# Performance work log

Measured on AMD Instinct MI355X. Metric: run time of the kernel, lower is better.

The kernel has to match this reference:

```python
import jax, jax.numpy as jnp
import numpy as np

B, S = 16, 8192
D_MODEL = 128          # config.moe_intermediate_size
D_HID = 512            # config.intermediate_size
N_EXPERTS = 8
BEH_DIM = 32           # config.behavior_embedding_dim
N_BEH = 16             # config.num_behavior -> embedding rows = N_BEH + 1


def setup_inputs() -> dict:
    key = jax.random.key(0)
    k1, k2, k3, k4, k5, k6 = jax.random.split(key, 6)
    hidden_states = jax.random.normal(k1, (B, S, D_MODEL), dtype=jnp.float32)
    position_index = jax.random.randint(k2, (B, S), 0, N_EXPERTS, dtype=jnp.int32)
    behavior_index = jax.random.randint(k3, (B, S), 0, N_BEH + 1, dtype=jnp.int32)
    din = D_MODEL + BEH_DIM
    # expert weights: wi maps (D_MODEL+BEH_DIM)->D_HID, wo maps D_HID->D_MODEL (no bias)
    Wi = jax.random.normal(k4, (N_EXPERTS, din, D_HID), dtype=jnp.float32) * (din ** -0.5)
    Wo = jax.random.normal(k5, (N_EXPERTS, D_HID, D_MODEL), dtype=jnp.float32) * (D_HID ** -0.5)
    emb = jax.random.normal(k6, (N_BEH + 1, BEH_DIM), dtype=jnp.float32)
    return {"hidden_states": hidden_states, "position_index": position_index,
            "behavior_index": behavior_index, "Wi": Wi, "Wo": Wo, "emb": emb}


def reference(hidden_states, position_index, behavior_index, Wi, Wo, emb):
    # behavior injection: concat learned behavior embedding onto each token
    x = jnp.concatenate([hidden_states, emb[behavior_index]], axis=-1)  # [B,S,Din]
    out = jnp.zeros_like(hidden_states)
    # sparse expert dispatch: each token routed to exactly one expert by position_index
    # (loop over small fixed expert count; dropout is identity at p=0 / eval)
    for e in range(Wi.shape[0]):
        h = jax.nn.relu(jnp.einsum('bsd,dh->bsh', x, Wi[e]))   # [B,S,H]
        y = jnp.einsum('bsh,hd->bsd', h, Wo[e])                # [B,S,D]
        out = out + jnp.where((position_index == e)[..., None], y, 0.0)
    return out
```

## Files before the change

kernel.cpp:

```cpp
#include <hip/hip_runtime.h>
#include <stdint.h>

typedef short bf16x8 __attribute__((ext_vector_type(8)));
typedef float f32x4 __attribute__((ext_vector_type(4)));
typedef float f32x16 __attribute__((ext_vector_type(16)));
typedef unsigned short ushort_t;
typedef ushort_t ushort8 __attribute__((ext_vector_type(8)));

#define TOKENS 131072
#define DMODEL 128
#define DIN 160
#define DHID 512
#define NEXP 8
#define BEH 32
#define CAP 24576
#define MT 64
#define TILES (CAP / MT)

#define OFF_COUNTS 0
#define OFF_LISTS  1024
#define OFF_WIP    (OFF_LISTS + NEXP*CAP*4)
#define OFF_WOP    (OFF_WIP + 8*16*10*64*8*2)

#define SCATTER_BLOCKS (TOKENS / 256)
#define NWI (8*16*10*64)
#define NWO (8*4*32*64)
#define PACK_BLOCKS ((NWI + NWO + 255) / 256)

#define STEP_SHORTS 9216

typedef const __attribute__((address_space(1))) uint32_t* gu32p;
typedef __attribute__((address_space(3))) uint32_t* lu32p;

__device__ __forceinline__ ushort_t f2b(float f) {
    union { float f; uint32_t u; } x; x.f = f;
    uint32_t r = x.u + 0x7FFF + ((x.u >> 16) & 1);
    return (ushort_t)(r >> 16);
}

__device__ __forceinline__ uint32_t pk2(float lo, float hi) {
    uint32_t a = __float_as_uint(lo) + 0x8000u;
    uint32_t b = __float_as_uint(hi) + 0x8000u;
    return (a >> 16) | (b & 0xFFFF0000u);
}

__global__ __launch_bounds__(256) void prep_kernel(
    const int* __restrict__ pos, int* __restrict__ counts, int* __restrict__ lists,
    const float* __restrict__ Wi, const float* __restrict__ Wo,
    ushort_t* __restrict__ wiP, ushort_t* __restrict__ woP)
{
    __shared__ int lcnt[NEXP];
    __shared__ int lbase[NEXP];
    int tid = threadIdx.x;
    if (blockIdx.x < SCATTER_BLOCKS) {
        if (tid < NEXP) lcnt[tid] = 0;
        __syncthreads();
        int t = blockIdx.x * 256 + tid;
        int e = pos[t];
        int slot = atomicAdd(&lcnt[e], 1);
        __syncthreads();
        if (tid < NEXP) lbase[tid] = atomicAdd(&counts[tid], lcnt[tid]);
        __syncthreads();
        int p = lbase[e] + slot;
        if (p < CAP) lists[e * CAP + p] = t;
        return;
    }
    int idx = (blockIdx.x - SCATTER_BLOCKS) * 256 + tid;
    if (idx < NWI) {
        int L = idx & 63; int r = idx >> 6;
        int f = r % 10; r /= 10;
        int step = r & 15; int e = r >> 4;
        int H = step * 32 + (L & 31);
        int kb = f * 16 + ((L >> 5) & 1) * 8;
        ushort8 o;
        #pragma unroll
        for (int j = 0; j < 8; ++j)
            o[j] = f2b(Wi[((size_t)e * DIN + kb + j) * DHID + H]);
        *(ushort8*)(wiP + (size_t)idx * 8) = o;
    } else {
        int i2 = idx - NWI;
        if (i2 >= NWO) return;
        int L = i2 & 63; int r = i2 >> 6;
        int sub = r & 31; r >>= 5;
        int n = r & 3; int e = r >> 2;
        int hb = sub * 16 + 4 * ((L >> 5) & 1);
        int dm = n * 32 + (L & 31);
        ushort8 o;
        #pragma unroll
        for (int j = 0; j < 8; ++j) {
            int H = hb + (j & 3) + 8 * (j >> 2);
            o[j] = f2b(Wo[((size_t)e * DHID + H) * DMODEL + dm]);
        }
        *(ushort8*)(woP + (size_t)i2 * 8) = o;
    }
}

__device__ __forceinline__ void stage_step(
    const ushort_t* __restrict__ wiPe, const ushort_t* __restrict__ woPe,
    ushort_t* dstBuf, int step, int tid)
{
    #pragma unroll
    for (int it = 0; it < 9; ++it) {
        int g = it * 128 + tid;
        const ushort_t* src;
        if (g < 640) {
            src = wiPe + (size_t)step * 5120 + (size_t)g * 8;
        } else {
            int g2 = g - 640;
            int n = g2 >> 7;
            src = woPe + (size_t)(n * 32 + 2 * step) * 512 + (size_t)(g2 & 127) * 8;
        }
        __builtin_amdgcn_global_load_lds((gu32p)(const void*)src,
                                         (lu32p)(void*)(dstBuf + g * 8), 16, 0, 0);
    }
}

__device__ __forceinline__ bf16x8 load_x8(const float* __restrict__ hidden,
                                          const float* __restrict__ emb,
                                          int t, int bi, int c0) {
    if (t < 0) return (bf16x8)0;
    const float* src = (c0 < DMODEL) ? (hidden + (size_t)t * DMODEL + c0)
                                     : (emb + (size_t)bi * BEH + (c0 - DMODEL));
    f32x4 p0 = *(const f32x4*)src;
    f32x4 p1 = *(const f32x4*)(src + 4);
    uint32_t d0 = pk2(p0[0], p0[1]), d1 = pk2(p0[2], p0[3]);
    uint32_t d2 = pk2(p1[0], p1[1]), d3 = pk2(p1[2], p1[3]);
    return __builtin_bit_cast(bf16x8, (uint4){d0, d1, d2, d3});
}

__global__ __launch_bounds__(128, 2) void expert_gemm(
    const float* __restrict__ hidden, const int* __restrict__ bindex,
    const int* __restrict__ lists, const int* __restrict__ counts,
    const ushort_t* __restrict__ wiP, const ushort_t* __restrict__ woP,
    const float* __restrict__ emb, float* __restrict__ out)
{
    int e = blockIdx.y;
    int tile = blockIdx.x;
    int count = counts[e]; if (count > CAP) count = CAP;
    int base = tile * MT;
    if (base >= count) return;
    int mvalid = count - base; if (mvalid > MT) mvalid = MT;

    __shared__ ushort_t wbuf[2][STEP_SHORTS];

    int tid = threadIdx.x;
    int lane = tid & 63;
    int w = tid >> 6;
    int l31 = lane & 31;
    int hi = lane >> 5;

    const int* listE = lists + (size_t)e * CAP + base;
    const ushort_t* wiPe = wiP + (size_t)e * 16 * 10 * 64 * 8;
    const ushort_t* woPe = woP + (size_t)e * 4 * 32 * 64 * 8;

    stage_step(wiPe, woPe, wbuf[0], 0, tid);

    bf16x8 xf[10];
    int row = w * 32 + l31;
    int tok = -1, bi = 0;
    if (row < mvalid) { tok = listE[row]; bi = bindex[tok]; }
    #pragma unroll
    for (int f = 0; f < 10; ++f)
        xf[f] = load_x8(hidden, emb, tok, bi, f * 16 + hi * 8);

    f32x16 yacc[4] = {};

    #pragma unroll 2
    for (int step = 0; step < 16; ++step) {
        int cur = step & 1;
        __syncthreads();
        if (step + 1 < 16)
            stage_step(wiPe, woPe, wbuf[cur ^ 1], step + 1, tid);

        const ushort_t* wiS = wbuf[cur];
        const ushort_t* woS = wbuf[cur] + 5120;

        f32x16 hacc = (f32x16)0;
        #pragma unroll
        for (int f = 0; f < 10; ++f) {
            bf16x8 a = *(const bf16x8*)&wiS[f * 512 + lane * 8];
            hacc = __builtin_amdgcn_mfma_f32_32x32x16_bf16(a, xf[f], hacc, 0, 0, 0);
        }

        #pragma unroll
        for (int sg = 0; sg < 2; ++sg) {
            float h[8];
            #pragma unroll
            for (int j = 0; j < 8; ++j) {
                float v = hacc[sg * 8 + j];
                h[j] = v > 0.f ? v : 0.f;
            }
            uint4 dv = { pk2(h[0], h[1]), pk2(h[2], h[3]),
                         pk2(h[4], h[5]), pk2(h[6], h[7]) };
            bf16x8 afrag = __builtin_bit_cast(bf16x8, dv);
            #pragma unroll
            for (int n = 0; n < 4; ++n) {
                bf16x8 b = *(const bf16x8*)&woS[(n * 2 + sg) * 512 + lane * 8];
                yacc[n] = __builtin_amdgcn_mfma_f32_32x32x16_bf16(afrag, b, yacc[n], 0, 0, 0);
            }
        }
    }

    #pragma unroll
    for (int reg = 0; reg < 16; ++reg) {
        int tr = (reg & 3) + 8 * (reg >> 2) + 4 * hi;
        int orow = w * 32 + tr;
        if (orow < mvalid) {
            int t = listE[orow];
            float* dst = out + (size_t)t * DMODEL + l31;
            #pragma unroll
            for (int n = 0; n < 4; ++n)
                dst[n * 32] = yacc[n][reg];
        }
    }
}

extern "C" void kernel_launch(void* const* d_in, const int* in_sizes, int n_in,
                              void* d_out, int out_size, void* d_ws, size_t ws_size,
                              hipStream_t stream) {
    const float* hidden = (const float*)d_in[0];
    const int*   pos    = (const int*)d_in[1];
    const int*   beh    = (const int*)d_in[2];
    const float* Wi     = (const float*)d_in[3];
    const float* Wo     = (const float*)d_in[4];
    const float* emb    = (const float*)d_in[5];

    char* ws = (char*)d_ws;
    int* counts   = (int*)(ws + OFF_COUNTS);
    int* lists    = (int*)(ws + OFF_LISTS);
    ushort_t* wiP = (ushort_t*)(ws + OFF_WIP);
    ushort_t* woP = (ushort_t*)(ws + OFF_WOP);

    hipMemsetAsync(counts, 0, NEXP * sizeof(int), stream);
    prep_kernel<<<SCATTER_BLOCKS + PACK_BLOCKS, 256, 0, stream>>>(pos, counts, lists, Wi, Wo, wiP, woP);
    expert_gemm<<<dim3(TILES, NEXP), 128, 0, stream>>>(
        hidden, beh, lists, counts, wiP, woP, emb, (float*)d_out);
}
```

Measured before the change: 90.90 us.

## Compact expert tile grid and split output columns across four waves per block

The 2D grid of CAP/MT tiles per expert, mostly empty blocks, is replaced by a 1D grid sized to the real tile count. Each block maps its index to an expert and tile through a prefix sum over counts. Blocks grow to 256 threads: two wave pairs share the 64-row tile and each wave computes half the output columns. This removes empty block launches and raises waves per block, but the first GEMM (hidden activations) is now computed twice per row tile, once by each column-half wave.

After: 100.4 us. 1.1x slower.

```diff
diff --git a/kernel.cpp b/kernel.cpp
--- a/kernel.cpp
+++ b/kernel.cpp
@@ -15,7 +15,8 @@
 #define BEH 32
 #define CAP 24576
 #define MT 64
-#define TILES (CAP / MT)
+
+#define GEMM_BLOCKS (TOKENS / MT + NEXP)
 
 #define OFF_COUNTS 0
 #define OFF_LISTS  1024
@@ -100,8 +101,9 @@
     ushort_t* dstBuf, int step, int tid)
 {
     #pragma unroll
-    for (int it = 0; it < 9; ++it) {
-        int g = it * 128 + tid;
+    for (int it = 0; it < 5; ++it) {
+        int g = it * 256 + tid;
+        if (it == 4 && tid >= 128) break;
         const ushort_t* src;
         if (g < 640) {
             src = wiPe + (size_t)step * 5120 + (size_t)g * 8;
@@ -128,17 +130,24 @@
     return __builtin_bit_cast(bf16x8, (uint4){d0, d1, d2, d3});
 }
 
-__global__ __launch_bounds__(128, 2) void expert_gemm(
+__global__ __launch_bounds__(256, 4) void expert_gemm(
     const float* __restrict__ hidden, const int* __restrict__ bindex,
     const int* __restrict__ lists, const int* __restrict__ counts,
     const ushort_t* __restrict__ wiP, const ushort_t* __restrict__ woP,
     const float* __restrict__ emb, float* __restrict__ out)
 {
-    int e = blockIdx.y;
-    int tile = blockIdx.x;
-    int count = counts[e]; if (count > CAP) count = CAP;
+    int bid = blockIdx.x;
+    int e = -1, tile = 0, count = 0;
+    int acc = 0;
+    #pragma unroll
+    for (int k = 0; k < NEXP; ++k) {
+        int c = counts[k]; if (c > CAP) c = CAP;
+        int t = (c + MT - 1) >> 6;
+        if (e < 0 && bid < acc + t) { e = k; tile = bid - acc; count = c; }
+        acc += t;
+    }
+    if (e < 0) return;
     int base = tile * MT;
-    if (base >= count) return;
     int mvalid = count - base; if (mvalid > MT) mvalid = MT;
 
     __shared__ ushort_t wbuf[2][STEP_SHORTS];
@@ -146,6 +155,8 @@
     int tid = threadIdx.x;
     int lane = tid & 63;
     int w = tid >> 6;
+    int tt = w & 1;
+    int nn = w >> 1;
     int l31 = lane & 31;
     int hi = lane >> 5;
 
@@ -156,14 +167,14 @@
     stage_step(wiPe, woPe, wbuf[0], 0, tid);
 
     bf16x8 xf[10];
-    int row = w * 32 + l31;
+    int row = tt * 32 + l31;
     int tok = -1, bi = 0;
     if (row < mvalid) { tok = listE[row]; bi = bindex[tok]; }
     #pragma unroll
     for (int f = 0; f < 10; ++f)
         xf[f] = load_x8(hidden, emb, tok, bi, f * 16 + hi * 8);
 
-    f32x16 yacc[4] = {};
+    f32x16 yacc[2] = {};
 
     #pragma unroll 2
     for (int step = 0; step < 16; ++step) {
@@ -194,9 +205,10 @@
                          pk2(h[4], h[5]), pk2(h[6], h[7]) };
             bf16x8 afrag = __builtin_bit_cast(bf16x8, dv);
             #pragma unroll
-            for (int n = 0; n < 4; ++n) {
+            for (int ni = 0; ni < 2; ++ni) {
+                int n = nn * 2 + ni;
                 bf16x8 b = *(const bf16x8*)&woS[(n * 2 + sg) * 512 + lane * 8];
-                yacc[n] = __builtin_amdgcn_mfma_f32_32x32x16_bf16(afrag, b, yacc[n], 0, 0, 0);
+                yacc[ni] = __builtin_amdgcn_mfma_f32_32x32x16_bf16(afrag, b, yacc[ni], 0, 0, 0);
             }
         }
     }
@@ -204,13 +216,12 @@
     #pragma unroll
     for (int reg = 0; reg < 16; ++reg) {
         int tr = (reg & 3) + 8 * (reg >> 2) + 4 * hi;
-        int orow = w * 32 + tr;
+        int orow = tt * 32 + tr;
         if (orow < mvalid) {
             int t = listE[orow];
-            float* dst = out + (size_t)t * DMODEL + l31;
-            #pragma unroll
-            for (int n = 0; n < 4; ++n)
-                dst[n * 32] = yacc[n][reg];
+            float* dst = out + (size_t)t * DMODEL + nn * 64 + l31;
+            dst[0]  = yacc[0][reg];
+            dst[32] = yacc[1][reg];
         }
     }
 }
@@ -233,6 +244,6 @@
 
     hipMemsetAsync(counts, 0, NEXP * sizeof(int), stream);
     prep_kernel<<<SCATTER_BLOCKS + PACK_BLOCKS, 256, 0, stream>>>(pos, counts, lists, Wi, Wo, wiP, woP);
-    expert_gemm<<<dim3(TILES, NEXP), 128, 0, stream>>>(
+    expert_gemm<<<GEMM_BLOCKS, 256, 0, stream>>>(
         hidden, beh, lists, counts, wiP, woP, emb, (float*)d_out);
 }
```
